# Kernel tuning notes

Measured on AMD Instinct MI355X. Metric: run time of the kernel, lower is better.

Reference implementation:

```python
import jax, jax.numpy as jnp
import numpy as np

SCALE = 64 ** 0.5  # hardcoded in original module regardless of dims


def setup_inputs() -> dict:
    key = jax.random.key(0)
    kx, kw = jax.random.split(key)
    B, S, D, O = 8, 2048, 512, 512
    x = jax.random.normal(kx, (B, S, D), dtype=jnp.float32)
    kernel = jax.random.normal(kw, (3, D, O), dtype=jnp.float32) * 0.02
    return {"x": x, "kernel": kernel}


def reference(x, kernel):
    # x: [B, S, D], kernel: [3, D, O]
    WQ = jnp.einsum('bsd,do->bso', x, kernel[0])
    WK = jnp.einsum('bsd,do->bso', x, kernel[1])
    WV = jnp.einsum('bsd,do->bso', x, kernel[2])
    QK = jnp.einsum('bso,bto->bst', WQ, WK)  # [B, S, S]
    # argmin of row-sums, taken from batch element 0 and applied to all batches
    # (faithful to c[0] in the original TF code)
    row_sums = jnp.sum(QK, axis=2)          # [B, S]
    c0 = jnp.argmin(row_sums[0])            # scalar index
    # Original removes row c0, scales, softmaxes remaining rows over last axis,
    # then re-inserts a zero row at c0. Softmax is row-independent, so this is
    # equivalent to softmax on all rows followed by zeroing row c0.
    A = jax.nn.softmax(QK / SCALE, axis=-1)  # [B, S, S]
    row_mask = (jnp.arange(QK.shape[1]) == c0)[None, :, None]
    A = jnp.where(row_mask, jnp.zeros((), A.dtype), A)
    V = jnp.einsum('bst,bto->bso', A, WV)    # [B, S, O]
    return V
```

## Files before the change

kernel.cpp:

```cpp
#include <hip/hip_runtime.h>
#include <stdint.h>

typedef __attribute__((ext_vector_type(8))) short short8;
typedef __attribute__((ext_vector_type(4))) float f32x4;

__device__ __forceinline__ float bf2f(unsigned short u) {
  union { unsigned int i; float f; } x; x.i = ((unsigned int)u) << 16; return x.f;
}
__device__ __forceinline__ unsigned short f2bf(float f) {
  union { float f; unsigned int i; } x; x.f = f;
  unsigned int u = x.i;
  unsigned int r = (u + 0x7FFFu + ((u >> 16) & 1u)) >> 16;
  return (unsigned short)r;
}
__device__ __forceinline__ unsigned int fmono(float f) {
  unsigned int u = __float_as_uint(f);
  return (u & 0x80000000u) ? ~u : (u | 0x80000000u);
}

typedef const __attribute__((address_space(1))) void* gas_ptr;
typedef __attribute__((address_space(3))) void* las_ptr;
__device__ __forceinline__ void gld_lds16(const void* g, void* l) {
  __builtin_amdgcn_global_load_lds((gas_ptr)g, (las_ptr)l, 16, 0, 0);
}

__global__ void cvt_kernel(const float* __restrict__ x, unsigned short* __restrict__ xbf,
                           const float* __restrict__ kern, unsigned short* __restrict__ wbfT) {
  int bid = blockIdx.x;
  if (bid < 4096) {
    int i = bid * 256 + threadIdx.x;
    const float4* xp = (const float4*)x;
    float4 a = xp[2 * i], b = xp[2 * i + 1];
    union { unsigned short us[8]; uint4 v; } o;
    o.us[0] = f2bf(a.x); o.us[1] = f2bf(a.y); o.us[2] = f2bf(a.z); o.us[3] = f2bf(a.w);
    o.us[4] = f2bf(b.x); o.us[5] = f2bf(b.y); o.us[6] = f2bf(b.z); o.us[7] = f2bf(b.w);
    ((uint4*)xbf)[i] = o.v;
  } else {
    __shared__ float tile[32][33];
    int b = bid - 4096;
    int w = b >> 8;
    int r2 = b & 255;
    int d0 = (r2 >> 4) * 32, o0 = (r2 & 15) * 32;
    int c = threadIdx.x & 31, r0 = threadIdx.x >> 5;
    const float* kp = kern + (size_t)w * 262144;
    unsigned short* op = wbfT + (size_t)w * 262144;
#pragma unroll
    for (int i = 0; i < 4; ++i)
      tile[r0 + 8 * i][c] = kp[(size_t)(d0 + r0 + 8 * i) * 512 + o0 + c];
    __syncthreads();
#pragma unroll
    for (int i = 0; i < 4; ++i)
      op[(size_t)(o0 + r0 + 8 * i) * 512 + d0 + c] = f2bf(tile[c][r0 + 8 * i]);
  }
}

template <int MODE, int BNT>
__global__ __launch_bounds__(512, 1) void gemm8p(
    const unsigned short* __restrict__ A, const unsigned short* __restrict__ B,
    void* __restrict__ C, int M, int N, int K,
    long long Abat, long long Bbat, long long Cbat, float scale,
    const unsigned long long* __restrict__ keyp) {
  constexpr int LB = BNT / 128;
  constexpr int BHB = (BNT / 2) * 128;
  constexpr int PBUF = 32768 + 2 * BHB;
  constexpr int WM = (BNT == 128) ? 4 : 2;
  constexpr int RPW = 256 / WM;
  constexpr int MF = RPW / 16;
  constexpr int IC = MF / 4;
  __shared__ __align__(16) char lds[2 * PBUF];

  const int tx = N / BNT, ty = M >> 8;
  const int nwg = gridDim.x;
  const int bid = blockIdx.x;
  const int swz = (bid & 7) * (nwg >> 3) + (bid >> 3);
  const int tpz = tx * ty;
  const int z = swz / tpz;
  const int rem = swz - z * tpz;
  const int by = rem / tx;
  const int bx = rem - by * tx;
  const unsigned short* Ab = A + (size_t)z * (size_t)Abat;
  const unsigned short* Bb = B + (size_t)z * (size_t)Bbat;
  const int bm0 = by << 8;
  const int bn0 = bx * BNT;

  const int tid = threadIdx.x, lane = tid & 63, w = tid >> 6;
  const int wr = (WM == 4) ? (w >> 1) : (w >> 2);
  const int wc = (WM == 4) ? (w & 1) : (w & 3);
  const int ln15 = lane & 15, hi = lane >> 4;
  const unsigned xorv = (unsigned)(lane & 7) << 4;
  const unsigned K2 = (unsigned)K * 2;

  const char* gsrc[4];
  gsrc[0] = (const char*)(Ab + (size_t)bm0 * K);
  gsrc[1] = (const char*)(Ab + (size_t)(bm0 + 128) * K);
  gsrc[2] = (const char*)(Bb + (size_t)bn0 * K);
  gsrc[3] = (const char*)(Bb + (size_t)(bn0 + BNT / 2) * K);
  const int hoff_[4] = {0, 16384, 32768, 32768 + BHB};
  unsigned op0 = (unsigned)(w * 1024 + lane * 16);
  unsigned op1 = op0 + 8192;
  const unsigned soff0 = (op0 >> 7) * K2 + ((op0 & 127) ^ (((op0 >> 7) & 7) << 4));
  const unsigned soff1 = (op1 >> 7) * K2 + ((op1 & 127) ^ (((op1 >> 7) & 7) << 4));
  const int lb0 = w * 1024, lb1 = 8192 + w * 1024;

#define STAGE(h, pp, kb)                                              \
  do {                                                                \
    char* lp_ = lds + (pp) * PBUF + hoff_[h];                         \
    const char* gp_ = gsrc[h] + ((unsigned)(kb) << 1);                \
    gld_lds16(gp_ + soff0, lp_ + lb0);                                \
    if ((h) < 2 || LB == 2) gld_lds16(gp_ + soff1, lp_ + lb1);        \
  } while (0)

  f32x4 acc[MF][4];
#pragma unroll
  for (int i = 0; i < MF; ++i)
#pragma unroll
    for (int j = 0; j < 4; ++j) acc[i][j] = (f32x4){0.f, 0.f, 0.f, 0.f};

  f32x4 accs1[MF];
  short8 onesf;
  if constexpr (MODE == 2) {
#pragma unroll
    for (int i = 0; i < MF; ++i) accs1[i] = (f32x4){0.f, 0.f, 0.f, 0.f};
#pragma unroll
    for (int j = 0; j < 8; ++j) onesf[j] = (short)0x3F80;
  }

  const int NT = K >> 6;
  STAGE(0, 0, 0);
  STAGE(1, 0, 0);
  STAGE(2, 0, 0);
  STAGE(3, 0, 0);
  asm volatile("s_waitcnt vmcnt(0)" ::: "memory");
  __builtin_amdgcn_s_barrier();

  short8 bfrag[4][2];
  for (int t = 0; t < NT; ++t) {
    const int p = t & 1;
    char* Lp = lds + p * PBUF;
    const int kN = (t + 1) << 6;
    const bool sN = (t + 1 < NT);
#pragma unroll
    for (int q = 0; q < 4; ++q) {
      if (q == 0) {
#pragma unroll
        for (int nf = 0; nf < 4; ++nf) {
          const int col = wc * 64 + nf * 16 + ln15;
          const char* bp = Lp + 32768 + ((col >= BNT / 2) ? BHB : 0) +
                           (col & (BNT / 2 - 1)) * 128;
#pragma unroll
          for (int k = 0; k < 2; ++k)
            bfrag[nf][k] = *(const short8*)(bp + (((unsigned)(k * 64 + hi * 16)) ^ xorv));
        }
      }
      short8 af[IC][2];
#pragma unroll
      for (int i = 0; i < IC; ++i) {
        const int row = wr * RPW + (q * IC + i) * 16 + ln15;
        const char* ap = Lp + ((row >> 7) << 14) + (row & 127) * 128;
#pragma unroll
        for (int k = 0; k < 2; ++k)
          af[i][k] = *(const short8*)(ap + (((unsigned)(k * 64 + hi * 16)) ^ xorv));
      }
      if (q == 0 && sN) { STAGE(0, p ^ 1, kN); STAGE(2, p ^ 1, kN); }
      if (q == 1 && sN) { STAGE(1, p ^ 1, kN); STAGE(3, p ^ 1, kN); }
      __builtin_amdgcn_s_setprio(1);
#pragma unroll
      for (int i = 0; i < IC; ++i) {
#pragma unroll
        for (int nf = 0; nf < 4; ++nf)
#pragma unroll
          for (int k = 0; k < 2; ++k)
            acc[q * IC + i][nf] = __builtin_amdgcn_mfma_f32_16x16x32_bf16(
                af[i][k], bfrag[nf][k], acc[q * IC + i][nf], 0, 0, 0);
        if constexpr (MODE == 2) {
#pragma unroll
          for (int k = 0; k < 2; ++k)
            accs1[q * IC + i] = __builtin_amdgcn_mfma_f32_16x16x32_bf16(
                af[i][k], onesf, accs1[q * IC + i], 0, 0, 0);
        }
      }
      __builtin_amdgcn_s_setprio(0);
    }
    asm volatile("s_waitcnt vmcnt(0) lgkmcnt(0)" ::: "memory");
    __builtin_amdgcn_s_barrier();
  }
#undef STAGE

  const int rg = hi * 4;
  const int cc = ln15;
  int c0 = 0;
  if constexpr (MODE == 2) c0 = (int)(unsigned int)(*keyp & 0xffffffffULL);
#pragma unroll
  for (int mf = 0; mf < MF; ++mf) {
#pragma unroll
    for (int nf = 0; nf < 4; ++nf) {
#pragma unroll
      for (int r = 0; r < 4; ++r) {
        int m = bm0 + wr * RPW + mf * 16 + rg + r;
        int n = bn0 + wc * 64 + nf * 16 + cc;
        float v = acc[mf][nf][r];
        if (MODE == 0) {
          ((unsigned short*)C)[(size_t)z * (size_t)Cbat + (size_t)m * N + n] =
              f2bf(__expf(v * scale));
        } else if (MODE == 1) {
          int bb = n >> 11, tl = n & 2047;
          ((unsigned short*)C)[((size_t)(bb * 512 + m) << 11) + tl] = f2bf(v);
        } else if (MODE == 2) {
          float lv = (m == c0) ? 0.f : (1.f / accs1[mf][r]);
          ((float*)C)[(size_t)z * (size_t)Cbat + (size_t)m * N + n] = v * lv;
        } else {
          size_t idx = (size_t)(n >> 9) * 8388608 + (size_t)m * 512 + (n & 511);
          float sc = (n >> 9) ? 1.0f : 0.125f;
          ((unsigned short*)C)[idx] = f2bf(v * sc);
        }
      }
    }
  }
}

__global__ void ksum_kernel(const unsigned short* __restrict__ WK, float* __restrict__ partial) {
  int col = threadIdx.x;
  int t0 = blockIdx.x * 64;
  float s = 0.f;
  for (int t = 0; t < 64; ++t) s += bf2f(WK[(size_t)(t0 + t) * 512 + col]);
  partial[blockIdx.x * 512 + col] = s;
}

__global__ void rs_argmin_kernel(const unsigned short* __restrict__ WQ,
                                 const float* __restrict__ partial,
                                 unsigned long long* __restrict__ key) {
  __shared__ __align__(16) float ks[512];
  int tid = threadIdx.x;
  for (int c = tid; c < 512; c += 256) {
    float s = 0.f;
#pragma unroll
    for (int j = 0; j < 32; ++j) s += partial[j * 512 + c];
    ks[c] = s;
  }
  __syncthreads();
  int w = tid >> 6, lane = tid & 63;
  float4 ka = *(const float4*)&ks[lane * 8];
  float4 kb = *(const float4*)&ks[lane * 8 + 4];
  for (int it = 0; it < 16; ++it) {
    int row = blockIdx.x * 64 + w * 16 + it;
    uint4 q = *(const uint4*)(WQ + (size_t)row * 512 + lane * 8);
    float d = 0.f;
    d += bf2f((unsigned short)(q.x & 0xffff)) * ka.x;
    d += bf2f((unsigned short)(q.x >> 16)) * ka.y;
    d += bf2f((unsigned short)(q.y & 0xffff)) * ka.z;
    d += bf2f((unsigned short)(q.y >> 16)) * ka.w;
    d += bf2f((unsigned short)(q.z & 0xffff)) * kb.x;
    d += bf2f((unsigned short)(q.z >> 16)) * kb.y;
    d += bf2f((unsigned short)(q.w & 0xffff)) * kb.z;
    d += bf2f((unsigned short)(q.w >> 16)) * kb.w;
#pragma unroll
    for (int m = 32; m; m >>= 1) d += __shfl_xor(d, m);
    if (lane == 0) {
      unsigned long long kk = ((unsigned long long)fmono(d) << 32) | (unsigned int)row;
      atomicMin(key, kk);
    }
  }
}

extern "C" void kernel_launch(void* const* d_in, const int* in_sizes, int n_in,
                              void* d_out, int out_size, void* d_ws, size_t ws_size,
                              hipStream_t stream) {
  const float* x = (const float*)d_in[0];
  const float* kern = (const float*)d_in[1];
  float* out = (float*)d_out;

  char* ws = (char*)d_ws;
  size_t off = 0;
  auto alloc = [&](size_t b) -> char* {
    char* p = ws + off;
    off += (b + 255) & ~(size_t)255;
    return p;
  };
  unsigned short* xbf = (unsigned short*)alloc(16384ull * 512 * 2);
  unsigned short* wbfT = (unsigned short*)alloc(3ull * 512 * 512 * 2);
  unsigned short* WQ = (unsigned short*)alloc(16384ull * 512 * 2);
  unsigned short* WK = (unsigned short*)alloc(16384ull * 512 * 2);
  unsigned short* VT = (unsigned short*)alloc(16384ull * 512 * 2);
  float* partial = (float*)alloc(32ull * 512 * 4);
  unsigned long long* key = (unsigned long long*)alloc(256);
  size_t fixed = off;
  size_t sbytes = 2048ull * 2048 * 2;
  int nb = 1;
  if (ws_size > fixed + sbytes) {
    size_t av = (ws_size - fixed) / sbytes;
    nb = av > 8 ? 8 : (int)av;
    if (nb < 1) nb = 1;
  }
  unsigned short* S = (unsigned short*)alloc(sbytes * (size_t)nb);

  hipMemsetAsync(key, 0xFF, 8, stream);

  cvt_kernel<<<4864, 256, 0, stream>>>(x, xbf, kern, wbfT);

  gemm8p<3, 256><<<256, 512, 0, stream>>>(xbf, wbfT, WQ, 16384, 1024, 512, 0, 0, 0, 1.0f,
                                          nullptr);
  gemm8p<1, 128><<<256, 512, 0, stream>>>(wbfT + 524288, xbf, VT, 512, 16384, 512, 0, 0, 0, 1.0f,
                                          nullptr);

  ksum_kernel<<<32, 512, 0, stream>>>(WK, partial);
  rs_argmin_kernel<<<32, 256, 0, stream>>>(WQ, partial, key);

  for (int b0 = 0; b0 < 8; b0 += nb) {
    int cb = (8 - b0) < nb ? (8 - b0) : nb;
    gemm8p<0, 256><<<64 * cb, 512, 0, stream>>>(
        WQ + (size_t)b0 * 2048 * 512, WK + (size_t)b0 * 2048 * 512, S,
        2048, 2048, 512, 2048ll * 512, 2048ll * 512, 2048ll * 2048, 1.0f,
        nullptr);
    gemm8p<2, 128><<<32 * cb, 512, 0, stream>>>(
        S, VT + (size_t)b0 * 512 * 2048, out + (size_t)b0 * 2048 * 512,
        2048, 512, 2048, 2048ll * 2048, 512ll * 2048, 2048ll * 512, 1.0f,
        key);
  }
}
```

Measured before the change: 167.1 us.

## Switch GEMMs to triple-buffered LDS pipeline with fixed 256x128 tiles

```diff
diff --git a/kernel.cpp b/kernel.cpp
--- a/kernel.cpp
+++ b/kernel.cpp
@@ -54,22 +54,16 @@
   }
 }
 
-template <int MODE, int BNT>
-__global__ __launch_bounds__(512, 1) void gemm8p(
+template <int MODE>
+__global__ __launch_bounds__(512, 1) void gemm3r(
     const unsigned short* __restrict__ A, const unsigned short* __restrict__ B,
     void* __restrict__ C, int M, int N, int K,
     long long Abat, long long Bbat, long long Cbat, float scale,
     const unsigned long long* __restrict__ keyp) {
-  constexpr int LB = BNT / 128;
-  constexpr int BHB = (BNT / 2) * 128;
-  constexpr int PBUF = 32768 + 2 * BHB;
-  constexpr int WM = (BNT == 128) ? 4 : 2;
-  constexpr int RPW = 256 / WM;
-  constexpr int MF = RPW / 16;
-  constexpr int IC = MF / 4;
-  __shared__ __align__(16) char lds[2 * PBUF];
-
-  const int tx = N / BNT, ty = M >> 8;
+  constexpr int PBUF = 49152;
+  __shared__ __align__(16) char lds[3 * PBUF];
+
+  const int tx = N >> 7, ty = M >> 8;
   const int nwg = gridDim.x;
   const int bid = blockIdx.x;
   const int swz = (bid & 7) * (nwg >> 3) + (bid >> 3);
@@ -81,11 +75,10 @@
   const unsigned short* Ab = A + (size_t)z * (size_t)Abat;
   const unsigned short* Bb = B + (size_t)z * (size_t)Bbat;
   const int bm0 = by << 8;
-  const int bn0 = bx * BNT;
+  const int bn0 = bx << 7;
 
   const int tid = threadIdx.x, lane = tid & 63, w = tid >> 6;
-  const int wr = (WM == 4) ? (w >> 1) : (w >> 2);
-  const int wc = (WM == 4) ? (w & 1) : (w & 3);
+  const int wr = w >> 1, wc = w & 1;
   const int ln15 = lane & 15, hi = lane >> 4;
   const unsigned xorv = (unsigned)(lane & 7) << 4;
   const unsigned K2 = (unsigned)K * 2;
@@ -94,95 +87,97 @@
   gsrc[0] = (const char*)(Ab + (size_t)bm0 * K);
   gsrc[1] = (const char*)(Ab + (size_t)(bm0 + 128) * K);
   gsrc[2] = (const char*)(Bb + (size_t)bn0 * K);
-  gsrc[3] = (const char*)(Bb + (size_t)(bn0 + BNT / 2) * K);
-  const int hoff_[4] = {0, 16384, 32768, 32768 + BHB};
+  gsrc[3] = (const char*)(Bb + (size_t)(bn0 + 64) * K);
+  const int hoff_[4] = {0, 16384, 32768, 40960};
   unsigned op0 = (unsigned)(w * 1024 + lane * 16);
   unsigned op1 = op0 + 8192;
   const unsigned soff0 = (op0 >> 7) * K2 + ((op0 & 127) ^ (((op0 >> 7) & 7) << 4));
   const unsigned soff1 = (op1 >> 7) * K2 + ((op1 & 127) ^ (((op1 >> 7) & 7) << 4));
   const int lb0 = w * 1024, lb1 = 8192 + w * 1024;
 
-#define STAGE(h, pp, kb)                                              \
+#define STAGE(h, slot, kb)                                            \
   do {                                                                \
-    char* lp_ = lds + (pp) * PBUF + hoff_[h];                         \
+    char* lp_ = lds + (slot) * PBUF + hoff_[h];                       \
     const char* gp_ = gsrc[h] + ((unsigned)(kb) << 1);                \
     gld_lds16(gp_ + soff0, lp_ + lb0);                                \
-    if ((h) < 2 || LB == 2) gld_lds16(gp_ + soff1, lp_ + lb1);        \
+    if ((h) < 2) gld_lds16(gp_ + soff1, lp_ + lb1);                   \
   } while (0)
 
-  f32x4 acc[MF][4];
-#pragma unroll
-  for (int i = 0; i < MF; ++i)
+  f32x4 acc[4][4];
+#pragma unroll
+  for (int i = 0; i < 4; ++i)
 #pragma unroll
     for (int j = 0; j < 4; ++j) acc[i][j] = (f32x4){0.f, 0.f, 0.f, 0.f};
 
-  f32x4 accs1[MF];
+  f32x4 accs1[4];
   short8 onesf;
   if constexpr (MODE == 2) {
 #pragma unroll
-    for (int i = 0; i < MF; ++i) accs1[i] = (f32x4){0.f, 0.f, 0.f, 0.f};
+    for (int i = 0; i < 4; ++i) accs1[i] = (f32x4){0.f, 0.f, 0.f, 0.f};
 #pragma unroll
     for (int j = 0; j < 8; ++j) onesf[j] = (short)0x3F80;
   }
 
   const int NT = K >> 6;
-  STAGE(0, 0, 0);
-  STAGE(1, 0, 0);
-  STAGE(2, 0, 0);
-  STAGE(3, 0, 0);
-  asm volatile("s_waitcnt vmcnt(0)" ::: "memory");
+  STAGE(0, 0, 0); STAGE(1, 0, 0); STAGE(2, 0, 0); STAGE(3, 0, 0);
+  if (NT > 1) {
+    STAGE(0, 1, 64); STAGE(1, 1, 64); STAGE(2, 1, 64); STAGE(3, 1, 64);
+    asm volatile("s_waitcnt vmcnt(6)" ::: "memory");
+  } else {
+    asm volatile("s_waitcnt vmcnt(0)" ::: "memory");
+  }
   __builtin_amdgcn_s_barrier();
 
   short8 bfrag[4][2];
+  int cur = 0;
   for (int t = 0; t < NT; ++t) {
-    const int p = t & 1;
-    char* Lp = lds + p * PBUF;
-    const int kN = (t + 1) << 6;
-    const bool sN = (t + 1 < NT);
+    char* Lp = lds + cur * PBUF;
+    int s2 = cur + 2; if (s2 >= 3) s2 -= 3;
+    const int kN2 = (t + 2) << 6;
+    const bool sN2 = (t + 2 < NT);
 #pragma unroll
     for (int q = 0; q < 4; ++q) {
       if (q == 0) {
 #pragma unroll
         for (int nf = 0; nf < 4; ++nf) {
           const int col = wc * 64 + nf * 16 + ln15;
-          const char* bp = Lp + 32768 + ((col >= BNT / 2) ? BHB : 0) +
-                           (col & (BNT / 2 - 1)) * 128;
+          const char* bp = Lp + 32768 + ((col >= 64) ? 8192 : 0) + (col & 63) * 128;
 #pragma unroll
           for (int k = 0; k < 2; ++k)
             bfrag[nf][k] = *(const short8*)(bp + (((unsigned)(k * 64 + hi * 16)) ^ xorv));
         }
       }
-      short8 af[IC][2];
-#pragma unroll
-      for (int i = 0; i < IC; ++i) {
-        const int row = wr * RPW + (q * IC + i) * 16 + ln15;
+      short8 af[2];
+      {
+        const int row = wr * 64 + q * 16 + ln15;
         const char* ap = Lp + ((row >> 7) << 14) + (row & 127) * 128;
 #pragma unroll
         for (int k = 0; k < 2; ++k)
-          af[i][k] = *(const short8*)(ap + (((unsigned)(k * 64 + hi * 16)) ^ xorv));
+          af[k] = *(const short8*)(ap + (((unsigned)(k * 64 + hi * 16)) ^ xorv));
       }
-      if (q == 0 && sN) { STAGE(0, p ^ 1, kN); STAGE(2, p ^ 1, kN); }
-      if (q == 1 && sN) { STAGE(1, p ^ 1, kN); STAGE(3, p ^ 1, kN); }
+      if (q == 0 && sN2) STAGE(0, s2, kN2);
+      if (q == 1 && sN2) STAGE(1, s2, kN2);
+      if (q == 2 && sN2) STAGE(2, s2, kN2);
+      if (q == 3 && sN2) STAGE(3, s2, kN2);
       __builtin_amdgcn_s_setprio(1);
 #pragma unroll
-      for (int i = 0; i < IC; ++i) {
-#pragma unroll
-        for (int nf = 0; nf < 4; ++nf)
-#pragma unroll
-          for (int k = 0; k < 2; ++k)
-            acc[q * IC + i][nf] = __builtin_amdgcn_mfma_f32_16x16x32_bf16(
-                af[i][k], bfrag[nf][k], acc[q * IC + i][nf], 0, 0, 0);
-        if constexpr (MODE == 2) {
-#pragma unroll
-          for (int k = 0; k < 2; ++k)
-            accs1[q * IC + i] = __builtin_amdgcn_mfma_f32_16x16x32_bf16(
-                af[i][k], onesf, accs1[q * IC + i], 0, 0, 0);
-        }
+      for (int nf = 0; nf < 4; ++nf)
+#pragma unroll
+        for (int k = 0; k < 2; ++k)
+          acc[q][nf] = __builtin_amdgcn_mfma_f32_16x16x32_bf16(
+              af[k], bfrag[nf][k], acc[q][nf], 0, 0, 0);
+      if constexpr (MODE == 2) {
+#pragma unroll
+        for (int k = 0; k < 2; ++k)
+          accs1[q] = __builtin_amdgcn_mfma_f32_16x16x32_bf16(
+              af[k], onesf, accs1[q], 0, 0, 0);
       }
       __builtin_amdgcn_s_setprio(0);
     }
-    asm volatile("s_waitcnt vmcnt(0) lgkmcnt(0)" ::: "memory");
+    if (sN2) { asm volatile("s_waitcnt vmcnt(6) lgkmcnt(0)" ::: "memory"); }
+    else     { asm volatile("s_waitcnt vmcnt(0) lgkmcnt(0)" ::: "memory"); }
     __builtin_amdgcn_s_barrier();
+    ++cur; if (cur >= 3) cur = 0;
   }
 #undef STAGE
 
@@ -191,12 +186,12 @@
   int c0 = 0;
   if constexpr (MODE == 2) c0 = (int)(unsigned int)(*keyp & 0xffffffffULL);
 #pragma unroll
-  for (int mf = 0; mf < MF; ++mf) {
+  for (int mf = 0; mf < 4; ++mf) {
 #pragma unroll
     for (int nf = 0; nf < 4; ++nf) {
 #pragma unroll
       for (int r = 0; r < 4; ++r) {
-        int m = bm0 + wr * RPW + mf * 16 + rg + r;
+        int m = bm0 + wr * 64 + mf * 16 + rg + r;
         int n = bn0 + wc * 64 + nf * 16 + cc;
         float v = acc[mf][nf][r];
         if (MODE == 0) {
@@ -297,21 +292,21 @@
 
   cvt_kernel<<<4864, 256, 0, stream>>>(x, xbf, kern, wbfT);
 
-  gemm8p<3, 256><<<256, 512, 0, stream>>>(xbf, wbfT, WQ, 16384, 1024, 512, 0, 0, 0, 1.0f,
-                                          nullptr);
-  gemm8p<1, 128><<<256, 512, 0, stream>>>(wbfT + 524288, xbf, VT, 512, 16384, 512, 0, 0, 0, 1.0f,
-                                          nullptr);
+  gemm3r<3><<<512, 512, 0, stream>>>(xbf, wbfT, WQ, 16384, 1024, 512, 0, 0, 0, 1.0f,
+                                     nullptr);
+  gemm3r<1><<<256, 512, 0, stream>>>(wbfT + 524288, xbf, VT, 512, 16384, 512, 0, 0, 0, 1.0f,
+                                     nullptr);
 
   ksum_kernel<<<32, 512, 0, stream>>>(WK, partial);
   rs_argmin_kernel<<<32, 256, 0, stream>>>(WQ, partial, key);
 
   for (int b0 = 0; b0 < 8; b0 += nb) {
     int cb = (8 - b0) < nb ? (8 - b0) : nb;
-    gemm8p<0, 256><<<64 * cb, 512, 0, stream>>>(
+    gemm3r<0><<<128 * cb, 512, 0, stream>>>(
         WQ + (size_t)b0 * 2048 * 512, WK + (size_t)b0 * 2048 * 512, S,
         2048, 2048, 512, 2048ll * 512, 2048ll * 512, 2048ll * 2048, 1.0f,
         nullptr);
-    gemm8p<2, 128><<<32 * cb, 512, 0, stream>>>(
+    gemm3r<2><<<32 * cb, 512, 0, stream>>>(
         S, VT + (size_t)b0 * 512 * 2048, out + (size_t)b0 * 2048 * 512,
         2048, 512, 2048, 2048ll * 2048, 512ll * 2048, 2048ll * 512, 1.0f,
         key);
```

Measured after the change: 176.8 us. 5.8% more time.
